# Optimization experiments

Measured on AMD Instinct MI355X. Metric: run time of the kernel, lower is better.

Reference implementation:

```python
import jax, jax.numpy as jnp
import numpy as np
import math

EPS_BN1 = 1e-3   # batch_norm1 eps
EPS_BNP = 1e-5   # predictor BN default eps


def conv1d(x, w, b=None, stride=1, padding=0, dilation=1):
    # x: (B, Cin, T), w: (Cout, Cin, K)
    out = jax.lax.conv_general_dilated(
        x, w, window_strides=(stride,), padding=[(padding, padding)],
        rhs_dilation=(dilation,), dimension_numbers=('NCH', 'OIH', 'NCH'))
    if b is not None:
        out = out + b[None, :, None]
    return out


def bn_eval(x, g, b, m, v, eps):
    scale = g / jnp.sqrt(v + eps)
    return (x - m[None, :, None]) * scale[None, :, None] + b[None, :, None]


def setup_inputs() -> dict:
    key = jax.random.key(0)
    ks = jax.random.split(key, 16)
    B, Cin, T = 16, 256, 4096
    Cout, P = 256, 32
    f32 = jnp.float32

    def n(k, shape, s):
        return s * jax.random.normal(k, shape, dtype=f32)

    inp = {
        'x': n(ks[0], (B, Cin, T), 1.0),
        'conv1_w': n(ks[1], (2 * Cout, Cin, 1), 0.06),
        'bn1_g': 1.0 + n(ks[2], (2 * Cout,), 0.1),
        'bn1_b': n(ks[3], (2 * Cout,), 0.1),
        'bn1_m': n(ks[4], (2 * Cout,), 0.1),
        'bn1_v': 1.0 + 0.1 * jax.random.uniform(ks[5], (2 * Cout,), dtype=f32),
        'conv1x1_w': n(ks[6], (1, Cin, 1), 0.06),
        'p0_w': n(ks[7], (P, 2, 31), 0.1),
        'p0_b': n(ks[8], (P,), 0.05),
        'p0bn_g': jnp.ones((P,), f32), 'p0bn_b': jnp.zeros((P,), f32),
        'p0bn_m': n(ks[9], (P,), 0.1),
        'p0bn_v': 1.0 + 0.1 * jax.random.uniform(ks[10], (P,), dtype=f32),
        'p1_w': n(ks[11], (P, P, 15), 0.05),
        'p1_b': n(ks[12], (P,), 0.05),
        'p1bn_g': jnp.ones((P,), f32), 'p1bn_b': jnp.zeros((P,), f32),
        'p1bn_m': n(ks[13], (P,), 0.1),
        'p1bn_v': 1.0 + 0.1 * jax.random.uniform(ks[14], (P,), dtype=f32),
        # last predictor conv: weight scaled by 0.01, bias = -log(2) (per __init__)
        'p2_w': 0.01 * n(ks[15], (2, P, 15), 0.05),
        'p2_b': jnp.array([-math.log(2.0), -math.log(2.0)], dtype=f32),
        'norm_mean': jnp.ones((1,), f32),  # registered buffer, eval renorm
    }
    return inp


def _forward(x, conv1_w, bn1_g, bn1_b, bn1_m, bn1_v, conv1x1_w,
             p0_w, p0_b, p0bn_g, p0bn_b, p0bn_m, p0bn_v,
             p1_w, p1_b, p1bn_g, p1bn_b, p1bn_m, p1bn_v,
             p2_w, p2_b, norm_mean):
    B, Cin, T = x.shape
    sg = jax.lax.stop_gradient

    # conv1 -> BN -> GLU(dim=1); dropout is identity in eval
    feat = bn_eval(conv1d(x, conv1_w), bn1_g, bn1_b, bn1_m, bn1_v, EPS_BN1)
    a, g = jnp.split(feat, 2, axis=1)
    feat = a * jax.nn.sigmoid(g)                     # (B, Cout, T)

    # predictor on [__x, __x^2]
    xx = conv1d(x, conv1x1_w)                        # (B, 1, T)
    h = jnp.concatenate([xx, xx * xx], axis=1)       # (B, 2, T)
    h = jax.nn.silu(bn_eval(conv1d(h, p0_w, p0_b, padding=15),
                            p0bn_g, p0bn_b, p0bn_m, p0bn_v, EPS_BNP))
    h = jax.nn.silu(bn_eval(conv1d(h, p1_w, p1_b, padding=7),
                            p1bn_g, p1bn_b, p1bn_m, p1bn_v, EPS_BNP))
    jumps = conv1d(h, p2_w, p2_b, padding=7)         # (B, 2, T)

    weights = jax.nn.sigmoid(jumps[:, 0, :])         # (B, T)
    moves = jax.nn.sigmoid(jumps[:, 1, :]) * norm_mean[0]  # eval: renorm = norm_mean
    row_renorm = jnp.maximum(jnp.mean(moves, axis=1), 1.0)
    moves = moves / row_renorm[:, None]

    features = jnp.transpose(feat, (0, 2, 1))        # (B, T, C)
    fw = features * weights[:, :, None]

    # big_pool: poses value = cumsum(moves); grad path = local window of 21 moves
    # (the k=1..20 shift loop adds grad-only terms). Window sum via cumsum diff.
    c = jnp.cumsum(moves, axis=1)
    win = c - jnp.pad(c, ((0, 0), (21, 0)))[:, :T]   # sum of moves[i-20..i]
    poses = sg(c) + win - sg(win)                    # (B, T)

    floors = jnp.floor(poses)
    ceils = floors + 1.0
    w1 = 1.0 - (poses - floors)                      # func = line: 1 - t
    w2 = 1.0 - (ceils - poses)

    # moves <= 1 (sigmoid * norm_mean=1 / row_renorm>=1) => ceils.max()+1 <= T+2
    L = T + 2                                        # static bound for out length
    C = features.shape[2]
    bidx = jnp.arange(B)[:, None]
    fi = floors.astype(jnp.int32)
    ci = fi + 1
    out = jnp.zeros((B, L, C), dtype=features.dtype)
    out = out.at[bidx, fi].add(w1[:, :, None] * fw)
    out = out.at[bidx, ci].add(w2[:, :, None] * fw)

    x_evs = jnp.transpose(out, (0, 2, 1))            # (B, C, L)
    pad = 15 - (L % 15)                              # F.pad(0, 15 - L % 15)
    return jnp.pad(x_evs, ((0, 0), (0, 0), (0, pad)))


def reference(x, conv1_w, bn1_g, bn1_b, bn1_m, bn1_v, conv1x1_w,
              p0_w, p0_b, p0bn_g, p0bn_b, p0bn_m, p0bn_v,
              p1_w, p1_b, p1bn_g, p1bn_b, p1bn_m, p1bn_v,
              p2_w, p2_b, norm_mean):
    return _forward(x, conv1_w, bn1_g, bn1_b, bn1_m, bn1_v, conv1x1_w,
                    p0_w, p0_b, p0bn_g, p0bn_b, p0bn_m, p0bn_v,
                    p1_w, p1_b, p1bn_g, p1bn_b, p1bn_m, p1bn_v,
                    p2_w, p2_b, norm_mean)
```

## Files before the change

### kernel.cpp

```cpp
#include <hip/hip_runtime.h>
#include <hip/hip_bf16.h>

#define BB   16
#define CIN  256
#define TN   4096
#define LOUT 4110
#define FTS  4224

typedef __attribute__((ext_vector_type(8))) short s16x8;
typedef __attribute__((ext_vector_type(4))) float f32x4;

__device__ __forceinline__ float fsig(float g) {
  return __builtin_amdgcn_rcpf(1.f + __expf(-g));
}


__global__ __launch_bounds__(256) void k0_prep(
    const float* __restrict__ conv1_w, const float* __restrict__ p0_w,
    const float* __restrict__ p1_w, const float* __restrict__ p2_w,
    const float* __restrict__ bn1_g, const float* __restrict__ bn1_b,
    const float* __restrict__ bn1_m, const float* __restrict__ bn1_v,
    const float* __restrict__ p0_b, const float* __restrict__ p0g,
    const float* __restrict__ p0bb, const float* __restrict__ p0m,
    const float* __restrict__ p0v,
    const float* __restrict__ p1_b, const float* __restrict__ p1g,
    const float* __restrict__ p1bb, const float* __restrict__ p1m,
    const float* __restrict__ p1v,
    short* __restrict__ wBpk, float4* __restrict__ bnp,
    float* __restrict__ wp0T, short* __restrict__ wp1M,
    short* __restrict__ wp2M, float2* __restrict__ bnp0,
    float2* __restrict__ bnp1) {
  int bid = blockIdx.x, tid = threadIdx.x;
  if (bid < 512) {
    int e = bid * 256 + tid;
    int i = e & 7, l = (e >> 3) & 63, ks = (e >> 9) & 7, n16 = e >> 12;
    int n = n16 * 16 + (l & 15);
    int j = n & 63;
    int co = (j < 32) ? ((n >> 6) * 32 + j) : (256 + (n >> 6) * 32 + (j - 32));
    int ci = ks * 32 + (l >> 4) * 8 + i;
    __hip_bfloat16 hv = __float2bfloat16(conv1_w[co * 256 + ci]);
    wBpk[e] = *(short*)&hv;
  } else {
    int idx = (bid - 512) * 256 + tid;
    if (idx < 1984) {
      int ch = idx & 31, rem = idx >> 5;
      int ic = rem / 31, k = rem % 31;
      wp0T[idx] = p0_w[(ch * 2 + ic) * 31 + k];
    }
    {
      int i = idx & 7, l = (idx >> 3) & 63, nf = (idx >> 9) & 1, koff = idx >> 10;
      int ch = nf * 16 + (l & 15), ic = (l >> 4) * 8 + i;
      __hip_bfloat16 hv = __float2bfloat16(p1_w[(ch * 32 + ic) * 15 + koff]);
      wp1M[idx] = *(short*)&hv;
    }
    if (idx < 7680) {
      int i = idx & 7, l = (idx >> 3) & 63, koff = idx >> 9;
      int n = l & 15, ic = (l >> 4) * 8 + i;
      float v = (n < 2) ? p2_w[(n * 32 + ic) * 15 + koff] : 0.f;
      __hip_bfloat16 hv = __float2bfloat16(v);
      wp2M[idx] = *(short*)&hv;
    }
    if (idx < 32) {
      int ch = idx;
      float sc = p0g[ch] * rsqrtf(p0v[ch] + 1e-5f);
      bnp0[ch] = make_float2(sc, (p0_b[ch] - p0m[ch]) * sc + p0bb[ch]);
    }
    if (idx >= 32 && idx < 64) {
      int ch = idx - 32;
      float sc = p1g[ch] * rsqrtf(p1v[ch] + 1e-5f);
      bnp1[ch] = make_float2(sc, (p1_b[ch] - p1m[ch]) * sc + p1bb[ch]);
    }
    if (idx < 256) {
      int c = idx;
      float sa = bn1_g[c] * rsqrtf(bn1_v[c] + 1e-3f);
      float ba = bn1_b[c] - bn1_m[c] * sa;
      float sg = bn1_g[c + 256] * rsqrtf(bn1_v[c + 256] + 1e-3f);
      float bg = bn1_b[c + 256] - bn1_m[c + 256] * sg;
      bnp[c] = make_float4(sa, ba, sg, bg);
    }
  }
}

__global__ __launch_bounds__(512, 4) void k1_mfma(
    const float* __restrict__ x, const float* __restrict__ w1x1,
    const short* __restrict__ wBpk, const float4* __restrict__ bnp,
    __hip_bfloat16* __restrict__ featT, float* __restrict__ xx) {
  int ty = blockIdx.x, b = blockIdx.y;
  int t0 = ty * 64;
  __shared__ __align__(16) unsigned int hb[64 * 132];
  __shared__ float xws[8][68];
  int tid = threadIdx.x;
  int l = tid & 63, wv = tid >> 6;
  int j = tid >> 4;
  int tc = tid & 15;
  int q = (tc >> 1) & 3;
  const float* xb = x + (size_t)b * (CIN * TN) + t0 + 4 * tc;
  float xxp[4] = {0.f, 0.f, 0.f, 0.f};
#pragma unroll
  for (int iter = 0; iter < 4; ++iter) {
    int C = j + 32 * iter;
    int ci = 2 * C;
    float4 f0 = *(const float4*)(xb + (size_t)ci * TN);
    float4 f1 = *(const float4*)(xb + (size_t)(ci + 1) * TN);
    float w0 = w1x1[ci], w1 = w1x1[ci + 1];
    unsigned int* dst = hb + (C ^ (q << 2));
    float fa[4] = {f0.x, f0.y, f0.z, f0.w};
    float fb[4] = {f1.x, f1.y, f1.z, f1.w};
#pragma unroll
    for (int r = 0; r < 4; ++r) {
      __hip_bfloat16 lo = __float2bfloat16(fa[r]);
      __hip_bfloat16 hi = __float2bfloat16(fb[r]);
      unsigned int pk = (unsigned int)(*(unsigned short*)&lo) |
                        ((unsigned int)(*(unsigned short*)&hi) << 16);
      dst[(4 * tc + r) * 132] = pk;
      xxp[r] = fmaf(w0, fa[r], fmaf(w1, fb[r], xxp[r]));
    }
  }
#pragma unroll
  for (int r = 0; r < 4; ++r) {
    xxp[r] += __shfl_xor(xxp[r], 16);
    xxp[r] += __shfl_xor(xxp[r], 32);
  }
  if (l < 16) {
#pragma unroll
    for (int r = 0; r < 4; ++r) xws[wv][4 * l + r] = xxp[r];
  }
  __syncthreads();
  if (tid < 64)
    xx[b * TN + t0 + tid] = ((xws[0][tid] + xws[1][tid]) + (xws[2][tid] + xws[3][tid])) +
                            ((xws[4][tid] + xws[5][tid]) + (xws[6][tid] + xws[7][tid]));

  int lr = l & 15, lk = l >> 4;
  const short* wrow = wBpk + (size_t)l * 8;
  f32x4 acc[4][4];
#pragma unroll
  for (int i = 0; i < 4; ++i)
#pragma unroll
    for (int n = 0; n < 4; ++n) acc[i][n] = (f32x4){0.f, 0.f, 0.f, 0.f};

#pragma unroll 2
  for (int ks = 0; ks < 8; ++ks) {
    s16x8 bf[4], af[4];
#pragma unroll
    for (int nf = 0; nf < 4; ++nf)
      bf[nf] = *(const s16x8*)(wrow + (size_t)(wv * 4 + nf) * 4096 + ks * 512);
#pragma unroll
    for (int mf = 0; mf < 4; ++mf) {
      int row = mf * 16 + lr;
      int grp = ks * 4 + lk;
      int qr = (row >> 3) & 3;
      af[mf] = *(const s16x8*)(hb + row * 132 + ((grp ^ qr) << 2));
    }
#pragma unroll
    for (int mf = 0; mf < 4; ++mf)
#pragma unroll
      for (int nf = 0; nf < 4; ++nf)
        acc[mf][nf] = __builtin_amdgcn_mfma_f32_16x16x32_bf16(
            af[mf], bf[nf], acc[mf][nf], 0, 0, 0);
  }

  int cb = wv * 32;
#pragma unroll
  for (int nf = 0; nf < 2; ++nf) {
    float4 bn = bnp[cb + nf * 16 + lr];
    int c = cb + nf * 16 + lr;
#pragma unroll
    for (int mf = 0; mf < 4; ++mf) {
#pragma unroll
      for (int r = 0; r < 4; ++r) {
        float a = acc[mf][nf][r], g = acc[mf][nf + 2][r];
        float av = fmaf(a, bn.x, bn.y);
        float gv = fmaf(g, bn.z, bn.w);
        float fv = av * fsig(gv);
        int t = t0 + mf * 16 + lk * 4 + r;
        featT[((size_t)b * TN + t) * 256 + c] = __float2bfloat16(fv);
      }
    }
  }
}

__global__ __launch_bounds__(512) void k2_pred(
    const float* __restrict__ xx,
    const float* __restrict__ wp0T, const float2* __restrict__ bnp0,
    const short* __restrict__ wp1M, const float2* __restrict__ bnp1,
    const short* __restrict__ wp2M, const float* __restrict__ p2_b,
    const float* __restrict__ norm_mean,
    float* __restrict__ wts, float* __restrict__ mvr) {
  int t0 = blockIdx.x * 128;
  int b = blockIdx.y;
  __shared__ float xin[2][192];
  __shared__ short h0T[160 * 40];
  __shared__ short h1T[144 * 40];
  int tid = threadIdx.x;
  for (int q = tid; q < 192; q += 512) {
    int t = t0 - 29 + q;
    float v = (q < 186 && t >= 0 && t < TN) ? xx[b * TN + t] : 0.f;
    xin[0][q] = v;
    xin[1][q] = v * v;
  }
  __syncthreads();
  {
    int ch = tid & 31, tq = tid >> 5;
    int i0 = tq * 12;
    if (i0 < 156) {
      float2 bb0 = bnp0[ch];
      float a0[12];
#pragma unroll
      for (int j = 0; j < 12; ++j) a0[j] = 0.f;
#pragma unroll
      for (int ic = 0; ic < 2; ++ic) {
        float rr[44];
#pragma unroll
        for (int q = 0; q < 11; ++q) {
          float4 t4 = *(const float4*)(&xin[ic][i0 + q * 4]);
          rr[q * 4 + 0] = t4.x; rr[q * 4 + 1] = t4.y;
          rr[q * 4 + 2] = t4.z; rr[q * 4 + 3] = t4.w;
        }
#pragma unroll
        for (int k = 0; k < 31; ++k) {
          float w = wp0T[(ic * 31 + k) * 32 + ch];
#pragma unroll
          for (int j = 0; j < 12; ++j) a0[j] = fmaf(w, rr[j + k], a0[j]);
        }
      }
#pragma unroll
      for (int j = 0; j < 12; ++j) {
        int i = i0 + j;
        if (i < 156) {
          float v = a0[j] * bb0.x + bb0.y;
          float h = v * fsig(v);
          __hip_bfloat16 hv = __float2bfloat16(h);
          h0T[i * 40 + ch] = *(short*)&hv;
        }
      }
    }
    if (tid < 128) h0T[(156 + (tid >> 5)) * 40 + (tid & 31)] = 0;
  }
  __syncthreads();
  int l = tid & 63, wv = tid >> 6;
  int lrow = l & 15, lk8 = (l >> 4) * 8;
  {
    f32x4 acc[2][2];
#pragma unroll
    for (int i = 0; i < 2; ++i)
#pragma unroll
      for (int j = 0; j < 2; ++j) acc[i][j] = (f32x4){0.f, 0.f, 0.f, 0.f};
    int nmf = (wv == 0) ? 2 : 1;
    for (int koff = 0; koff < 15; ++koff) {
      const short* bp = wp1M + koff * 1024;
      s16x8 bf0 = *(const s16x8*)(bp + l * 8);
      s16x8 bf1 = *(const s16x8*)(bp + 512 + l * 8);
      for (int mi = 0; mi < nmf; ++mi) {
        int mf = (mi == 0) ? wv : 8;
        s16x8 af = *(const s16x8*)(&h0T[(mf * 16 + koff + lrow) * 40 + lk8]);
        acc[mi][0] = __builtin_amdgcn_mfma_f32_16x16x32_bf16(af, bf0, acc[mi][0], 0, 0, 0);
        acc[mi][1] = __builtin_amdgcn_mfma_f32_16x16x32_bf16(af, bf1, acc[mi][1], 0, 0, 0);
      }
    }
    for (int mi = 0; mi < nmf; ++mi) {
      int mf = (mi == 0) ? wv : 8;
#pragma unroll
      for (int nf = 0; nf < 2; ++nf) {
        int ch = nf * 16 + lrow;
        float2 bb = bnp1[ch];
#pragma unroll
        for (int r = 0; r < 4; ++r) {
          int row = mf * 16 + (l >> 4) * 4 + r;
          float v = acc[mi][nf][r] * bb.x + bb.y;
          float h = v * fsig(v);
          __hip_bfloat16 hv = __float2bfloat16(h);
          h1T[row * 40 + ch] = *(short*)&hv;
        }
      }
    }
  }
  __syncthreads();
  {
    f32x4 acc2 = (f32x4){0.f, 0.f, 0.f, 0.f};
    for (int koff = 0; koff < 15; ++koff) {
      s16x8 bf = *(const s16x8*)(wp2M + koff * 512 + l * 8);
      s16x8 af = *(const s16x8*)(&h1T[(wv * 16 + koff + lrow) * 40 + lk8]);
      acc2 = __builtin_amdgcn_mfma_f32_16x16x32_bf16(af, bf, acc2, 0, 0, 0);
    }
    int ch = lrow;
    if (ch < 2) {
      float pb = p2_b[ch];
      float nm = norm_mean[0];
#pragma unroll
      for (int r = 0; r < 4; ++r) {
        int t = t0 + wv * 16 + (l >> 4) * 4 + r;
        float a = acc2[r] + pb;
        float s = fsig(a);
        if (ch == 0) wts[b * TN + t] = s;
        else         mvr[b * TN + t] = s * nm;
      }
    }
  }
}

__global__ __launch_bounds__(256) void k3_scan(const float* __restrict__ mvr,
                                               float* __restrict__ poses,
                                               int* __restrict__ firstT) {
  int b = blockIdx.x, tid = threadIdx.x;
  __shared__ float stage[4096];
  __shared__ float wsum[4];
  __shared__ int shlast;
  for (int i = tid; i < 4096; i += 256) stage[i] = mvr[b * TN + i];
  __syncthreads();
  float v[16];
  float run = 0.f;
#pragma unroll
  for (int j = 0; j < 16; ++j) { run += stage[tid * 16 + j]; v[j] = run; }
  int l = tid & 63, wv = tid >> 6;
  float s = run;
#pragma unroll
  for (int off = 1; off < 64; off <<= 1) {
    float t = __shfl_up(s, off);
    if (l >= off) s += t;
  }
  if (l == 63) wsum[wv] = s;
  __syncthreads();
  float wpre = 0.f;
  for (int w2 = 0; w2 < wv; ++w2) wpre += wsum[w2];
  float incl = wpre + s;
  float total = wsum[0] + wsum[1] + wsum[2] + wsum[3];
  float excl = incl - run;
  float rn = total * (1.0f / 4096.0f);
  float inv = (rn > 1.0f) ? 1.0f / rn : 1.0f;
  float p16[16];
  float* pd = poses + b * TN + tid * 16;
#pragma unroll
  for (int j = 0; j < 16; ++j) { p16[j] = (excl + v[j]) * inv; pd[j] = p16[j]; }
  stage[tid] = p16[15];
  __syncthreads();
  int* ft = firstT + b * FTS;
  int prevf = (tid == 0) ? -1 : min((int)floorf(stage[tid - 1]), 4220);
  int f = prevf;
#pragma unroll
  for (int j = 0; j < 16; ++j) {
    f = min((int)floorf(p16[j]), 4220);
    for (int li = prevf + 1; li <= f; ++li) ft[li] = tid * 16 + j;
    prevf = f;
  }
  if (tid == 255) shlast = f;
  __syncthreads();
  for (int li = shlast + 1 + tid; li < FTS; li += 256) ft[li] = TN;
}

__global__ __launch_bounds__(256) void k4_gather(
    const __hip_bfloat16* __restrict__ featT, const float* __restrict__ wts,
    const float* __restrict__ poses, const int* __restrict__ firstT,
    float* __restrict__ out) {
  int d = blockIdx.x + 257 * blockIdx.y;
  int w = (d & 7) * 514 + (d >> 3);
  int lx = w % 257, b = w / 257;
  int l0 = lx * 16;
  __shared__ float acc[16][259];
  int tid = threadIdx.x;
  for (int i = tid; i < 16 * 259; i += 256) ((float*)acc)[i] = 0.f;
  const int* ft = firstT + b * FTS;
  int ts = (l0 == 0) ? 0 : ft[l0 - 1];
  int te = ft[l0 + 16];
  __syncthreads();
  int c = tid;
  if (ts < te) {
    const float* pp = poses + b * TN;
    const float* wp = wts + b * TN;
    const __hip_bfloat16* fp = featT + (size_t)(b * TN) * 256 + c;
    float p_cur = pp[ts];
    float w_cur = wp[ts];
    float f_cur = __bfloat162float(fp[(size_t)ts * 256]);
    float S_lo = 0.f, S_hi = 0.f;
    int cur = (int)floorf(p_cur);
    for (int t = ts; t < te; ++t) {
      float p_nxt = 0.f, w_nxt = 0.f, f_nxt = 0.f;
      if (t + 1 < te) {
        p_nxt = pp[t + 1];
        w_nxt = wp[t + 1];
        f_nxt = __bfloat162float(fp[(size_t)(t + 1) * 256]);
      }
      int fi = (int)floorf(p_cur);
      if (fi < cur) fi = cur;
      if (fi != cur) {
        int r = cur - l0;
        if (r >= 0 && r < 16) acc[r][c] = S_lo;
        if (fi == cur + 1) {
          S_lo = S_hi;
        } else {
          int r2 = cur + 1 - l0;
          if (r2 >= 0 && r2 < 16) acc[r2][c] = S_hi;
          S_lo = 0.f;
        }
        S_hi = 0.f;
        cur = fi;
      }
      float w2 = p_cur - (float)fi;
      float fw = f_cur * w_cur;
      S_lo = fmaf(1.f - w2, fw, S_lo);
      S_hi = fmaf(w2, fw, S_hi);
      p_cur = p_nxt; w_cur = w_nxt; f_cur = f_nxt;
    }
    int r = cur - l0;
    if (r >= 0 && r < 16) acc[r][c] = S_lo;
    int r2 = cur + 1 - l0;
    if (r2 >= 0 && r2 < 16) acc[r2][c] = S_hi;
  }
  __syncthreads();
  for (int i = tid; i < 4096; i += 256) {
    int c2 = i >> 4, r = i & 15;
    int l = l0 + r;
    if (l < LOUT) out[((size_t)b * 256 + c2) * LOUT + l] = acc[r][c2];
  }
}

extern "C" void kernel_launch(void* const* d_in, const int* in_sizes, int n_in,
                              void* d_out, int out_size, void* d_ws, size_t ws_size,
                              hipStream_t stream) {
  const float* x       = (const float*)d_in[0];
  const float* conv1_w = (const float*)d_in[1];
  const float* bn1_g   = (const float*)d_in[2];
  const float* bn1_b   = (const float*)d_in[3];
  const float* bn1_m   = (const float*)d_in[4];
  const float* bn1_v   = (const float*)d_in[5];
  const float* w1x1    = (const float*)d_in[6];
  const float* p0_w    = (const float*)d_in[7];
  const float* p0_b    = (const float*)d_in[8];
  const float* p0g     = (const float*)d_in[9];
  const float* p0bb    = (const float*)d_in[10];
  const float* p0m     = (const float*)d_in[11];
  const float* p0v     = (const float*)d_in[12];
  const float* p1_w    = (const float*)d_in[13];
  const float* p1_b    = (const float*)d_in[14];
  const float* p1g     = (const float*)d_in[15];
  const float* p1bb    = (const float*)d_in[16];
  const float* p1m     = (const float*)d_in[17];
  const float* p1v     = (const float*)d_in[18];
  const float* p2_w    = (const float*)d_in[19];
  const float* p2_b    = (const float*)d_in[20];
  const float* nmean   = (const float*)d_in[21];

  char* ws = (char*)d_ws;
  __hip_bfloat16* featT = (__hip_bfloat16*)ws;
  short* wBpk   = (short*)(ws + 33554432);
  float4* bnp   = (float4*)(ws + 33816576);
  float* wp0T   = (float*)(ws + 33820672);
  short* wp1M   = (short*)(ws + 33828864);
  short* wp2M   = (short*)(ws + 33859584);
  float2* bnp0  = (float2*)(ws + 33874944);
  float2* bnp1  = (float2*)(ws + 33875200);
  float* xx     = (float*)(ws + 33890304);
  float* wts    = (float*)(ws + 34152448);
  float* mvr    = (float*)(ws + 34414592);
  float* poses  = (float*)(ws + 34676736);
  int*   firstT = (int*)  (ws + 34938880);
  float* out    = (float*)d_out;

  k0_prep<<<dim3(572), dim3(256), 0, stream>>>(
      conv1_w, p0_w, p1_w, p2_w, bn1_g, bn1_b, bn1_m, bn1_v,
      p0_b, p0g, p0bb, p0m, p0v, p1_b, p1g, p1bb, p1m, p1v,
      wBpk, bnp, wp0T, wp1M, wp2M, bnp0, bnp1);
  k1_mfma<<<dim3(64, 16), dim3(512), 0, stream>>>(x, w1x1, wBpk, bnp, featT, xx);
  k2_pred<<<dim3(32, 16), dim3(512), 0, stream>>>(xx, wp0T, bnp0, wp1M, bnp1,
                                                  wp2M, p2_b, nmean, wts, mvr);
  k3_scan<<<dim3(16), dim3(256), 0, stream>>>(mvr, poses, firstT);
  k4_gather<<<dim3(257, 16), dim3(256), 0, stream>>>(featT, wts, poses, firstT, out);
}
```

Before: 90.41 us.

## Split predictor conv0 into separate kernel writing h0 to global scratch

Moves the first predictor convolution out of k2_pred into its own kernel, k2a_p0. It writes SiLU-activated bf16 h0 for all timesteps to a scratch buffer, which aliases the output buffer. The second kernel then loads h0 with halo rows from global memory instead of recomputing the overlapping halo per block. Padding positions are filled with the activation of the bias value. This removes the redundant halo recompute and the idle-thread imbalance in the conv0 phase, at the cost of an extra kernel launch and a global memory round-trip.

```diff
diff --git a/kernel.cpp b/kernel.cpp
--- a/kernel.cpp
+++ b/kernel.cpp
@@ -179,62 +179,77 @@
   }
 }
 
-__global__ __launch_bounds__(512) void k2_pred(
-    const float* __restrict__ xx,
-    const float* __restrict__ wp0T, const float2* __restrict__ bnp0,
+__global__ __launch_bounds__(512) void k2a_p0(
+    const float* __restrict__ xx, const float* __restrict__ wp0T,
+    const float2* __restrict__ bnp0, short* __restrict__ h0g) {
+  int t0 = blockIdx.x * 128;
+  int b = blockIdx.y;
+  __shared__ float xin[2][160];
+  int tid = threadIdx.x;
+  for (int q = tid; q < 160; q += 512) {
+    int t = t0 - 15 + q;
+    float v = (q < 158 && t >= 0 && t < TN) ? xx[b * TN + t] : 0.f;
+    xin[0][q] = v;
+    xin[1][q] = v * v;
+  }
+  __syncthreads();
+  int ch = tid & 31, tq = tid >> 5;
+  int i0 = tq * 8;
+  float2 bb0 = bnp0[ch];
+  float a0[8];
+#pragma unroll
+  for (int j = 0; j < 8; ++j) a0[j] = 0.f;
+#pragma unroll
+  for (int ic = 0; ic < 2; ++ic) {
+    float rr[40];
+#pragma unroll
+    for (int q = 0; q < 10; ++q) {
+      float4 t4 = *(const float4*)(&xin[ic][i0 + q * 4]);
+      rr[q * 4 + 0] = t4.x; rr[q * 4 + 1] = t4.y;
+      rr[q * 4 + 2] = t4.z; rr[q * 4 + 3] = t4.w;
+    }
+#pragma unroll
+    for (int k = 0; k < 31; ++k) {
+      float w = wp0T[(ic * 31 + k) * 32 + ch];
+#pragma unroll
+      for (int j = 0; j < 8; ++j) a0[j] = fmaf(w, rr[j + k], a0[j]);
+    }
+  }
+#pragma unroll
+  for (int j = 0; j < 8; ++j) {
+    float v = a0[j] * bb0.x + bb0.y;
+    float h = v * fsig(v);
+    __hip_bfloat16 hv = __float2bfloat16(h);
+    h0g[((size_t)b * TN + t0 + i0 + j) * 32 + ch] = *(short*)&hv;
+  }
+}
+
+__global__ __launch_bounds__(512) void k2b_pred(
+    const short* __restrict__ h0g, const float2* __restrict__ bnp0,
     const short* __restrict__ wp1M, const float2* __restrict__ bnp1,
     const short* __restrict__ wp2M, const float* __restrict__ p2_b,
     const float* __restrict__ norm_mean,
     float* __restrict__ wts, float* __restrict__ mvr) {
   int t0 = blockIdx.x * 128;
   int b = blockIdx.y;
-  __shared__ float xin[2][192];
   __shared__ short h0T[160 * 40];
   __shared__ short h1T[144 * 40];
   int tid = threadIdx.x;
-  for (int q = tid; q < 192; q += 512) {
-    int t = t0 - 29 + q;
-    float v = (q < 186 && t >= 0 && t < TN) ? xx[b * TN + t] : 0.f;
-    xin[0][q] = v;
-    xin[1][q] = v * v;
-  }
-  __syncthreads();
   {
-    int ch = tid & 31, tq = tid >> 5;
-    int i0 = tq * 12;
-    if (i0 < 156) {
-      float2 bb0 = bnp0[ch];
-      float a0[12];
-#pragma unroll
-      for (int j = 0; j < 12; ++j) a0[j] = 0.f;
-#pragma unroll
-      for (int ic = 0; ic < 2; ++ic) {
-        float rr[44];
-#pragma unroll
-        for (int q = 0; q < 11; ++q) {
-          float4 t4 = *(const float4*)(&xin[ic][i0 + q * 4]);
-          rr[q * 4 + 0] = t4.x; rr[q * 4 + 1] = t4.y;
-          rr[q * 4 + 2] = t4.z; rr[q * 4 + 3] = t4.w;
-        }
-#pragma unroll
-        for (int k = 0; k < 31; ++k) {
-          float w = wp0T[(ic * 31 + k) * 32 + ch];
-#pragma unroll
-          for (int j = 0; j < 12; ++j) a0[j] = fmaf(w, rr[j + k], a0[j]);
-        }
-      }
-#pragma unroll
-      for (int j = 0; j < 12; ++j) {
-        int i = i0 + j;
-        if (i < 156) {
-          float v = a0[j] * bb0.x + bb0.y;
-          float h = v * fsig(v);
-          __hip_bfloat16 hv = __float2bfloat16(h);
-          h0T[i * 40 + ch] = *(short*)&hv;
-        }
-      }
-    }
-    if (tid < 128) h0T[(156 + (tid >> 5)) * 40 + (tid & 31)] = 0;
+    int chf = tid & 31;
+    float vb = bnp0[chf].y;
+    float hbf = vb * fsig(vb);
+    __hip_bfloat16 hbv = __float2bfloat16(hbf);
+    short hbias = *(short*)&hbv;
+    for (int idx = tid; idx < 160 * 32; idx += 512) {
+      int row = idx >> 5;
+      int t = t0 - 14 + row;
+      short val;
+      if (row >= 156) val = 0;
+      else if (t >= 0 && t < TN) val = h0g[((size_t)b * TN + t) * 32 + chf];
+      else val = hbias;
+      h0T[row * 40 + chf] = val;
+    }
   }
   __syncthreads();
   int l = tid & 63, wv = tid >> 6;
@@ -454,14 +469,16 @@
   float* poses  = (float*)(ws + 34676736);
   int*   firstT = (int*)  (ws + 34938880);
   float* out    = (float*)d_out;
+  short* h0g    = (short*)d_out;
 
   k0_prep<<<dim3(572), dim3(256), 0, stream>>>(
       conv1_w, p0_w, p1_w, p2_w, bn1_g, bn1_b, bn1_m, bn1_v,
       p0_b, p0g, p0bb, p0m, p0v, p1_b, p1g, p1bb, p1m, p1v,
       wBpk, bnp, wp0T, wp1M, wp2M, bnp0, bnp1);
   k1_mfma<<<dim3(64, 16), dim3(512), 0, stream>>>(x, w1x1, wBpk, bnp, featT, xx);
-  k2_pred<<<dim3(32, 16), dim3(512), 0, stream>>>(xx, wp0T, bnp0, wp1M, bnp1,
-                                                  wp2M, p2_b, nmean, wts, mvr);
+  k2a_p0<<<dim3(32, 16), dim3(512), 0, stream>>>(xx, wp0T, bnp0, h0g);
+  k2b_pred<<<dim3(32, 16), dim3(512), 0, stream>>>(h0g, bnp0, wp1M, bnp1,
+                                                   wp2M, p2_b, nmean, wts, mvr);
   k3_scan<<<dim3(16), dim3(256), 0, stream>>>(mvr, poses, firstT);
   k4_gather<<<dim3(257, 16), dim3(256), 0, stream>>>(featT, wts, poses, firstT, out);
 }
```

Result: slower. 94.82 us (+4.9%).
